# Kernel optimization log

Hardware: AMD Instinct MI355X
Metric: run time of the kernel (lower is better)

## Reference

```python
import jax, jax.numpy as jnp
import numpy as np

N_NODES = 50000
N_EDGES = 1200000
N_REL = 40
N_BASES = 30
EMB = 64
HID = 128
N_GRAPHS = 64


def rgcn_layer(h, src, dst, edge_type, comp, basis, root, bias):
    # W_r = sum_b comp[r,b] * basis[b]  -> [R, in, out]
    W = jnp.einsum('rb,bio->rio', comp, basis)
    n = h.shape[0]
    # aggregate source features per (target node, relation): mean aggregation (PyG RGCNConv default)
    seg = dst * N_REL + edge_type                      # [E]
    msgs = h[src]                                      # [E, in]  (gather)
    agg = jax.ops.segment_sum(msgs, seg, num_segments=n * N_REL)
    agg = agg.reshape(n, N_REL, -1)                    # [N, R, in]
    cnt = jax.ops.segment_sum(jnp.ones((src.shape[0],), h.dtype), seg,
                              num_segments=n * N_REL).reshape(n, N_REL, 1)
    agg = agg / jnp.maximum(cnt, 1.0)
    out = jnp.einsum('nri,rio->no', agg, W) + h @ root + bias
    return out


def setup_inputs() -> dict:
    key = jax.random.key(0)
    ks = jax.random.split(key, 12)
    x = jnp.arange(N_NODES, dtype=jnp.int64) if jax.config.jax_enable_x64 else jnp.arange(N_NODES, dtype=jnp.int32)
    edge_index = jax.random.randint(ks[0], (2, N_EDGES), 0, N_NODES)
    edge_type = jax.random.randint(ks[1], (N_EDGES,), 0, N_REL)
    batch = jnp.sort(jax.random.randint(ks[2], (N_NODES,), 0, N_GRAPHS))
    s = 0.05
    node_emb = jax.random.normal(ks[3], (N_NODES, EMB), jnp.float32)
    comp1 = jax.random.normal(ks[4], (N_REL, N_BASES), jnp.float32) * s
    basis1 = jax.random.normal(ks[5], (N_BASES, EMB, HID), jnp.float32) * s
    root1 = jax.random.normal(ks[6], (EMB, HID), jnp.float32) * s
    bias1 = jnp.zeros((HID,), jnp.float32)
    comp2 = jax.random.normal(ks[7], (N_REL, N_BASES), jnp.float32) * s
    basis2 = jax.random.normal(ks[8], (N_BASES, HID, HID), jnp.float32) * s
    root2 = jax.random.normal(ks[9], (HID, HID), jnp.float32) * s
    bias2 = jnp.zeros((HID,), jnp.float32)
    return {"x": x, "edge_index": edge_index, "edge_type": edge_type, "batch": batch,
            "node_emb": node_emb,
            "comp1": comp1, "basis1": basis1, "root1": root1, "bias1": bias1,
            "comp2": comp2, "basis2": basis2, "root2": root2, "bias2": bias2}


def reference(x, edge_index, edge_type, batch, node_emb,
              comp1, basis1, root1, bias1, comp2, basis2, root2, bias2):
    src, dst = edge_index[0], edge_index[1]
    h = node_emb[x]                                              # embedding lookup
    h = jax.nn.relu(rgcn_layer(h, src, dst, edge_type, comp1, basis1, root1, bias1))
    h = jax.nn.relu(rgcn_layer(h, src, dst, edge_type, comp2, basis2, root2, bias2))
    # global mean pool over graphs in batch
    sums = jax.ops.segment_sum(h, batch, num_segments=N_GRAPHS)  # [G, HID]
    cnts = jax.ops.segment_sum(jnp.ones((h.shape[0],), h.dtype), batch,
                               num_segments=N_GRAPHS)[:, None]
    return sums / jnp.maximum(cnts, 1.0)
```

## Files before the change

### kernel.cpp

```cpp
#include <hip/hip_runtime.h>


#define N_NODES 50000
#define N_EDGES 1200000
#define N_REL   40
#define N_BASES 30
#define EMB     64
#define HID     128
#define N_GRAPHS 64

#define NKEY      320
#define PERM_CAP  ((size_t)N_EDGES + (size_t)NKEY * 256)
#define SP_EPB    1024

typedef float f32x4  __attribute__((ext_vector_type(4)));
typedef short bf16x8 __attribute__((ext_vector_type(8)));

__device__ __forceinline__ unsigned short f2bf(float x) {
    unsigned int u = __float_as_uint(x);
    u = (u + 0x7FFFu + ((u >> 16) & 1u)) >> 16;
    return (unsigned short)u;
}
__device__ __forceinline__ float bflo(unsigned int u) { return __uint_as_float(u << 16); }
__device__ __forceinline__ float bfhi(unsigned int u) { return __uint_as_float(u & 0xffff0000u); }

#define OFF_WF1   ((size_t)0)
#define OFF_WF2   ((size_t)163840)
#define OFF_CNT   ((size_t)491520)
#define OFF_H1    ((size_t)2491520)
#define OFF_H2    ((size_t)8891520)
#define OFF_HB1   ((size_t)15291520)
#define OFF_HB2   ((size_t)16891520)
#define OFF_CNTG  ((size_t)20091520)
#define OFF_POOL  ((size_t)20091584)
#define OFF_PSRC  ((size_t)20099776)
#define OFF_POS   ((size_t)21381696)
#define OFF_PDST  ((size_t)22663616)
#define OFF_HCR   ((size_t)23945536)
#define OFF_CCR   ((size_t)23945856)
#define OFF_POCR  ((size_t)23946176)
#define OFF_HD    ((size_t)23946560)
#define OFF_CD    ((size_t)23996560)
#define OFF_POD   ((size_t)24046560)
#define OFF_RF1   ((size_t)24096576)
#define OFF_RF2   ((size_t)24100672)
#define OFF_BREL  ((size_t)24108864)
#define OFF_PM    ((size_t)24110912)

template <int IN, int KT>
__global__ void k_Wfrag(const float* __restrict__ comp, const float* __restrict__ basis,
                        unsigned short* __restrict__ Wf) {
    const int FR = IN * HID;
    int idx = blockIdx.x * blockDim.x + threadIdx.x;
    if (idx >= N_REL * FR) return;
    int r = idx / FR, F = idx - r * FR;
    int j = F & 7, lane = (F >> 3) & 63, tt = F >> 9;
    int kt = tt % KT, ct = tt / KT;
    int k = kt * 32 + (lane >> 4) * 8 + j;
    int c = ct * 16 + (lane & 15);
    float s = 0.f;
#pragma unroll
    for (int b = 0; b < N_BASES; ++b)
        s += comp[r * N_BASES + b] * basis[((size_t)b * IN + k) * HID + c];
    Wf[idx] = f2bf(s);
}

template <int IN, int KT>
__global__ void k_rootfrag(const float* __restrict__ root, unsigned short* __restrict__ rf) {
    int idx = blockIdx.x * blockDim.x + threadIdx.x;
    if (idx >= IN * HID) return;
    int j = idx & 7, lane = (idx >> 3) & 63, tt = idx >> 9;
    int kt = tt % KT, ct = tt / KT;
    int k = kt * 32 + (lane >> 4) * 8 + j;
    int c = ct * 16 + (lane & 15);
    rf[idx] = f2bf(root[k * HID + c]);
}

__global__ void k_count(const int* __restrict__ dst, const int* __restrict__ etype,
                        float* __restrict__ cnt_t) {
    int e = blockIdx.x * blockDim.x + threadIdx.x;
    if (e >= N_EDGES) return;
    atomicAdd(&cnt_t[(size_t)etype[e] * N_NODES + dst[e]], 1.0f);
}

__global__ void k_deg_inv(float* __restrict__ cnt_t, int* __restrict__ hist) {
    int n = blockIdx.x * blockDim.x + threadIdx.x;
    if (n >= N_NODES) return;
    float s = 0.f;
#pragma unroll 8
    for (int r = 0; r < N_REL; ++r) {
        float c = cnt_t[(size_t)r * N_NODES + n];
        s += c;
        cnt_t[(size_t)r * N_NODES + n] = 1.0f / fmaxf(c, 1.0f);
    }
    hist[n] = (int)(s + 0.5f);
}

__global__ void k_scan_d(const int* __restrict__ hist, int* __restrict__ po) {
    __shared__ int csum[256];
    int t = threadIdx.x;
    const int CH = (N_NODES + 255) / 256;
    int k0 = t * CH, k1 = min(k0 + CH, N_NODES);
    int s = 0;
    for (int k = k0; k < k1; ++k) s += hist[k];
    csum[t] = s;
    __syncthreads();
    if (t == 0) {
        int acc = 0;
        for (int i = 0; i < 256; ++i) { int v = csum[i]; csum[i] = acc; acc += v; }
        po[N_NODES] = acc;
    }
    __syncthreads();
    int base = csum[t];
    for (int k = k0; k < k1; ++k) { po[k] = base; base += hist[k]; }
}

__global__ void k_hist_cr(const int* __restrict__ src, const int* __restrict__ dst,
                          const int* __restrict__ etype, int* __restrict__ hist,
                          int chn, int slc, int sdiv) {
    __shared__ int lh[NKEY];
    for (int t = threadIdx.x; t < NKEY; t += 256) lh[t] = 0;
    __syncthreads();
    int e = blockIdx.x * blockDim.x + threadIdx.x;
    if (e < N_EDGES) {
        int key = (dst[e] / chn) * (N_REL * slc) + etype[e] * slc + src[e] / sdiv;
        atomicAdd(&lh[key], 1);
    }
    __syncthreads();
    for (int t = threadIdx.x; t < NKEY; t += 256)
        if (lh[t]) atomicAdd(&hist[t], lh[t]);
}

__global__ void k_scan_cr(const int* __restrict__ hist, int* __restrict__ po) {
    if (threadIdx.x == 0) {
        int acc = 0;
        for (int k = 0; k < NKEY; ++k) {
            po[k] = acc;
            acc += ((hist[k] + 255) >> 8) << 8;
        }
        po[NKEY] = acc;
    }
}

__global__ void k_brel(const int* __restrict__ po, unsigned char* __restrict__ brel,
                       int slc) {
    int k = blockIdx.x * blockDim.x + threadIdx.x;
    if (k >= NKEY) return;
    unsigned char r = (unsigned char)((k % (N_REL * slc)) / slc);
    for (int b = po[k] >> 8; b < (po[k + 1] >> 8); ++b) brel[b] = r;
}

__global__ void k_fillpads(const int* __restrict__ hist, const int* __restrict__ po,
                           int* __restrict__ ps_src, int* __restrict__ ps_os,
                           int* __restrict__ ps_dst, int dumprow) {
    int k = blockIdx.x;
    int start = po[k] + hist[k], end = po[k + 1];
    for (int s = start + threadIdx.x; s < end; s += blockDim.x) {
        ps_src[s] = 0;
        ps_os[s] = dumprow;
        ps_dst[s] = 0;
    }
}

__global__ void k_scatter_s(const int* __restrict__ src, const int* __restrict__ dst,
                            const int* __restrict__ etype,
                            const int* __restrict__ po_cr, int* __restrict__ cur_cr,
                            const int* __restrict__ po_d, int* __restrict__ cur_d,
                            int* __restrict__ ps_src, int* __restrict__ ps_os,
                            int* __restrict__ ps_dst, int chn, int slc, int sdiv) {
    __shared__ int lh[NKEY], sbase[NKEY];
    int t = threadIdx.x;
    for (int k = t; k < NKEY; k += 256) lh[k] = 0;
    __syncthreads();
    int e0 = blockIdx.x * SP_EPB;
    int e_[4], key_[4];
#pragma unroll
    for (int i = 0; i < 4; ++i) {
        int e = e0 + t + i * 256;
        e_[i] = e;
        if (e < N_EDGES) {
            key_[i] = (dst[e] / chn) * (N_REL * slc) + etype[e] * slc + src[e] / sdiv;
            atomicAdd(&lh[key_[i]], 1);
        }
    }
    __syncthreads();
    for (int k = t; k < NKEY; k += 256) {
        if (lh[k]) sbase[k] = atomicAdd(&cur_cr[k], lh[k]);
        lh[k] = 0;
    }
    __syncthreads();
#pragma unroll
    for (int i = 0; i < 4; ++i) {
        if (e_[i] < N_EDGES) {
            int e = e_[i], key = key_[i];
            int d = dst[e];
            int p = atomicAdd(&lh[key], 1);
            int slot = po_cr[key] + sbase[key] + p;
            int os_g = po_d[d] + atomicAdd(&cur_d[d], 1);
            int os_l = os_g - po_d[(d / chn) * chn];
            ps_src[slot] = src[e];
            ps_os[slot] = os_l;
            ps_dst[slot] = d;
        }
    }
}

template <int IN, int KT>
__global__ __launch_bounds__(256, 4)
void k_rootgemm(const unsigned short* __restrict__ hb_in,
                const unsigned short* __restrict__ rf,
                const float* __restrict__ bias, float* __restrict__ h) {
    __shared__ unsigned short Wl[8 * KT * 64 * 8];
    {
        const f32x4* Wg = (const f32x4*)rf;
        f32x4* Wd = (f32x4*)Wl;
        for (int kk = threadIdx.x; kk < 8 * KT * 64; kk += 256) Wd[kk] = Wg[kk];
    }
    __syncthreads();

    int l = threadIdx.x & 63, wv = threadIdx.x >> 6;
    int lrow = l & 15, lk = l >> 4;
    int nbase = blockIdx.x * 64 + wv * 16;

    int nrow = min(nbase + lrow, N_NODES - 1);
    bf16x8 a[KT];
    const unsigned short* hrow = hb_in + (size_t)nrow * IN + lk * 8;
#pragma unroll
    for (int kt = 0; kt < KT; ++kt)
        a[kt] = *(const bf16x8*)(hrow + kt * 32);

    f32x4 acc[8];
#pragma unroll
    for (int ct = 0; ct < 8; ++ct) acc[ct] = (f32x4){0.f, 0.f, 0.f, 0.f};
#pragma unroll
    for (int ct = 0; ct < 8; ++ct) {
#pragma unroll
        for (int kt = 0; kt < KT; ++kt) {
            bf16x8 bb = *(const bf16x8*)(Wl + ((ct * KT + kt) * 64 + l) * 8);
            acc[ct] = __builtin_amdgcn_mfma_f32_16x16x32_bf16(a[kt], bb, acc[ct], 0, 0, 0);
        }
    }
#pragma unroll
    for (int q = 0; q < 4; ++q) {
        int n = nbase + lk * 4 + q;
        if (n < N_NODES) {
#pragma unroll
            for (int ct = 0; ct < 8; ++ct)
                h[(size_t)n * HID + ct * 16 + lrow] = acc[ct][q] + bias[ct * 16 + lrow];
        }
    }
}

template <int IN, int KT>
__global__ __launch_bounds__(256, 4)
void k_msg(const unsigned short* __restrict__ hb_in, const int* __restrict__ ps_src,
           const int* __restrict__ ps_os, const int* __restrict__ ps_dst,
           const float* __restrict__ invc_t, const int* __restrict__ pob, int nbk,
           const unsigned char* __restrict__ brel,
           const unsigned short* __restrict__ Wf, unsigned int* __restrict__ pm) {
    __shared__ unsigned short Wl[8 * KT * 64 * 8];
    int slot0 = pob[0] + blockIdx.x * 256;
    if (slot0 >= pob[nbk]) return;
    int r = brel[slot0 >> 8];

    {
        const f32x4* Wg = (const f32x4*)(Wf + (size_t)r * (8 * KT * 64 * 8));
        f32x4* Wd = (f32x4*)Wl;
        for (int kk = threadIdx.x; kk < 8 * KT * 64; kk += 256) Wd[kk] = Wg[kk];
    }
    __syncthreads();

    int l = threadIdx.x & 63, wv = threadIdx.x >> 6;
    int lrow = l & 15, lk = l >> 4;
    const float* invr = invc_t + (size_t)r * N_NODES;

    for (int t = wv; t < 16; t += 4) {
        int slot = slot0 + t * 16 + lrow;
        int sv = ps_src[slot];
        int os = ps_os[slot];
        int d  = ps_dst[slot];
        float inv = invr[d];

        bf16x8 a[KT];
        const unsigned short* hrow = hb_in + (size_t)sv * IN + lk * 8;
#pragma unroll
        for (int kt = 0; kt < KT; ++kt)
            a[kt] = *(const bf16x8*)(hrow + kt * 32);

        f32x4 acc[8];
#pragma unroll
        for (int ct = 0; ct < 8; ++ct) acc[ct] = (f32x4){0.f, 0.f, 0.f, 0.f};
#pragma unroll
        for (int ct = 0; ct < 8; ++ct) {
#pragma unroll
            for (int kt = 0; kt < KT; ++kt) {
                bf16x8 bb = *(const bf16x8*)(Wl + ((ct * KT + kt) * 64 + l) * 8);
                acc[ct] = __builtin_amdgcn_mfma_f32_16x16x32_bf16(a[kt], bb, acc[ct], 0, 0, 0);
            }
        }
#pragma unroll
        for (int q = 0; q < 4; ++q) {
            int row = lk * 4 + q;
            int osq   = __shfl(os, row);
            float ivq = __shfl(inv, row);
            unsigned int* dp = pm + (size_t)osq * 64 + lrow;
#pragma unroll
            for (int cp = 0; cp < 4; ++cp) {
                unsigned int u = (unsigned int)f2bf(acc[2 * cp][q] * ivq)
                               | ((unsigned int)f2bf(acc[2 * cp + 1][q] * ivq) << 16);
                dp[cp * 16] = u;
            }
        }
    }
}

template <bool WRITE_HB>
__global__ __launch_bounds__(256, 8)
void k_reduce(const unsigned int* __restrict__ pm, const int* __restrict__ po_d,
              int n0chunk, int chn, float* __restrict__ h,
              unsigned short* __restrict__ hb_out) {
    int wv = threadIdx.x >> 6, p = threadIdx.x & 63;
    int n = n0chunk + blockIdx.x * 4 + wv;
    if (n >= n0chunk + chn) return;
    int pmbase = po_d[n0chunk];
    int b0 = po_d[n] - pmbase;
    int cn = po_d[n + 1] - pmbase - b0;
    float lo = 0.f, hi = 0.f;
    const unsigned int* rp = pm + (size_t)b0 * 64 + p;
    int k = 0;
    for (; k + 4 <= cn; k += 4) {
        unsigned int u0 = rp[0], u1 = rp[64], u2 = rp[128], u3 = rp[192];
        rp += 256;
        lo += bflo(u0) + bflo(u1) + bflo(u2) + bflo(u3);
        hi += bfhi(u0) + bfhi(u1) + bfhi(u2) + bfhi(u3);
    }
    for (; k < cn; ++k) {
        unsigned int u = rp[0];
        rp += 64;
        lo += bflo(u); hi += bfhi(u);
    }
    int cA = (p & 15) + 32 * (p >> 4);
    float* hp = h + (size_t)n * HID;
    float vA = fmaxf(hp[cA] + lo, 0.f);
    float vB = fmaxf(hp[cA + 16] + hi, 0.f);
    hp[cA] = vA;
    hp[cA + 16] = vB;
    if (WRITE_HB) {
        hb_out[(size_t)n * HID + cA] = f2bf(vA);
        hb_out[(size_t)n * HID + cA + 16] = f2bf(vB);
    }
}

__global__ void k_cvt_emb(const float* __restrict__ emb, const int* __restrict__ x,
                          unsigned short* __restrict__ hb) {
    int idx = blockIdx.x * blockDim.x + threadIdx.x;
    if (idx >= N_NODES * (EMB / 4)) return;
    int n = idx / (EMB / 4), c4 = idx % (EMB / 4);
    int row = x[n];
    float4 v = *(const float4*)(emb + (size_t)row * EMB + c4 * 4);
    ushort4 o = {f2bf(v.x), f2bf(v.y), f2bf(v.z), f2bf(v.w)};
    *(ushort4*)(hb + (size_t)n * EMB + c4 * 4) = o;
}

__global__ void k_gcount2(const int* __restrict__ batch, float* __restrict__ cntG) {
    int g = threadIdx.x;
    if (g >= N_GRAPHS) return;
    int lo = 0, hi = N_NODES;
    while (lo < hi) { int m = (lo + hi) >> 1; if (batch[m] < g) lo = m + 1; else hi = m; }
    int lb0 = lo;
    lo = 0; hi = N_NODES;
    while (lo < hi) { int m = (lo + hi) >> 1; if (batch[m] < g + 1) lo = m + 1; else hi = m; }
    cntG[g] = (float)(lo - lb0);
}

__global__ void k_pool(const float* __restrict__ h, const int* __restrict__ batch,
                       float* __restrict__ acc) {
    const int CH = 64;
    int n0 = blockIdx.x * CH;
    int o = threadIdx.x;
    int nend = min(n0 + CH, N_NODES);
    if (n0 >= N_NODES) return;
    int curg = batch[n0];
    float run = 0.f;
    for (int n = n0; n < nend; ++n) {
        int g = batch[n];
        if (g != curg) {
            atomicAdd(&acc[(size_t)curg * HID + o], run);
            run = 0.f;
            curg = g;
        }
        run += h[(size_t)n * HID + o];
    }
    atomicAdd(&acc[(size_t)curg * HID + o], run);
}

__global__ void k_final(const float* __restrict__ acc, const float* __restrict__ cntG,
                        float* __restrict__ out) {
    int idx = blockIdx.x * blockDim.x + threadIdx.x;
    if (idx >= N_GRAPHS * HID) return;
    int g = idx >> 7;
    out[idx] = acc[idx] / fmaxf(cntG[g], 1.0f);
}

extern "C" void kernel_launch(void* const* d_in, const int* in_sizes, int n_in,
                              void* d_out, int out_size, void* d_ws, size_t ws_size,
                              hipStream_t stream) {
    const int*   x         = (const int*)d_in[0];
    const int*   edge_index= (const int*)d_in[1];
    const int*   etype     = (const int*)d_in[2];
    const int*   batch     = (const int*)d_in[3];
    const float* node_emb  = (const float*)d_in[4];
    const float* comp1     = (const float*)d_in[5];
    const float* basis1    = (const float*)d_in[6];
    const float* root1     = (const float*)d_in[7];
    const float* bias1     = (const float*)d_in[8];
    const float* comp2     = (const float*)d_in[9];
    const float* basis2    = (const float*)d_in[10];
    const float* root2     = (const float*)d_in[11];
    const float* bias2     = (const float*)d_in[12];
    float* out = (float*)d_out;

    const int* src = edge_index;
    const int* dst = edge_index + N_EDGES;

    float* ws = (float*)d_ws;
    unsigned short* Wf1 = (unsigned short*)(ws + OFF_WF1);
    unsigned short* Wf2 = (unsigned short*)(ws + OFF_WF2);
    float* cnt_t = ws + OFF_CNT;
    float* h1   = ws + OFF_H1;
    float* h2   = ws + OFF_H2;
    unsigned short* hb1 = (unsigned short*)(ws + OFF_HB1);
    unsigned short* hb2 = (unsigned short*)(ws + OFF_HB2);
    float* cntG = ws + OFF_CNTG;
    float* pool = ws + OFF_POOL;
    int*   ps_src = (int*)(ws + OFF_PSRC);
    int*   ps_os  = (int*)(ws + OFF_POS);
    int*   ps_dst = (int*)(ws + OFF_PDST);
    int*   hist_cr = (int*)(ws + OFF_HCR);
    int*   cur_cr  = (int*)(ws + OFF_CCR);
    int*   po_cr   = (int*)(ws + OFF_POCR);
    int*   hist_d  = (int*)(ws + OFF_HD);
    int*   cur_d   = (int*)(ws + OFF_CD);
    int*   po_d    = (int*)(ws + OFF_POD);
    unsigned short* rf1 = (unsigned short*)(ws + OFF_RF1);
    unsigned short* rf2 = (unsigned short*)(ws + OFF_RF2);
    unsigned char* brel = (unsigned char*)(ws + OFF_BREL);
    unsigned int* pm = (unsigned int*)(ws + OFF_PM);

    size_t ws_floats = ws_size / sizeof(float);
    int nch = 4;
    if (ws_floats >= OFF_PM + ((size_t)N_EDGES / 1 + 12504) * 64) nch = 1;
    else if (ws_floats >= OFF_PM + ((size_t)N_EDGES / 2 + 12504) * 64) nch = 2;
    int chn = N_NODES / nch;
    int slc = 8 / nch;
    int sdiv = 6250 * nch;
    int nbk = NKEY / nch;
    int capr = N_EDGES / nch + 12504;
    int gridm = (capr + NKEY * 256 / nch) / 256 + 2;

    hipMemsetAsync(cnt_t, 0, (size_t)N_NODES * N_REL * sizeof(float), stream);
    hipMemsetAsync(cntG, 0, (size_t)(N_GRAPHS + N_GRAPHS * HID) * sizeof(float), stream);
    hipMemsetAsync(hist_cr, 0, 2 * NKEY * sizeof(int), stream);
    hipMemsetAsync(cur_d, 0, N_NODES * sizeof(int), stream);

    k_count<<<(N_EDGES + 255) / 256, 256, 0, stream>>>(dst, etype, cnt_t);
    k_deg_inv<<<(N_NODES + 255) / 256, 256, 0, stream>>>(cnt_t, hist_d);
    k_scan_d<<<1, 256, 0, stream>>>(hist_d, po_d);
    k_hist_cr<<<(N_EDGES + 255) / 256, 256, 0, stream>>>(src, dst, etype, hist_cr,
                                                         chn, slc, sdiv);
    k_scan_cr<<<1, 64, 0, stream>>>(hist_cr, po_cr);
    k_brel<<<2, 256, 0, stream>>>(po_cr, brel, slc);
    k_fillpads<<<NKEY, 256, 0, stream>>>(hist_cr, po_cr, ps_src, ps_os, ps_dst, capr - 1);
    k_scatter_s<<<(N_EDGES + SP_EPB - 1) / SP_EPB, 256, 0, stream>>>(
        src, dst, etype, po_cr, cur_cr, po_d, cur_d, ps_src, ps_os, ps_dst,
        chn, slc, sdiv);

    k_Wfrag<EMB, 2><<<(N_REL * EMB * HID + 255) / 256, 256, 0, stream>>>(comp1, basis1, Wf1);
    k_Wfrag<HID, 4><<<(N_REL * HID * HID + 255) / 256, 256, 0, stream>>>(comp2, basis2, Wf2);
    k_rootfrag<EMB, 2><<<(EMB * HID + 255) / 256, 256, 0, stream>>>(root1, rf1);
    k_rootfrag<HID, 4><<<(HID * HID + 255) / 256, 256, 0, stream>>>(root2, rf2);

    k_cvt_emb<<<(N_NODES * (EMB / 4) + 255) / 256, 256, 0, stream>>>(node_emb, x, hb1);
    k_rootgemm<EMB, 2><<<(N_NODES + 63) / 64, 256, 0, stream>>>(hb1, rf1, bias1, h1);
    for (int c = 0; c < nch; ++c) {
        k_msg<EMB, 2><<<gridm, 256, 0, stream>>>(hb1, ps_src, ps_os, ps_dst, cnt_t,
                                                 po_cr + c * nbk, nbk, brel, Wf1, pm);
        k_reduce<true><<<chn / 4, 256, 0, stream>>>(pm, po_d, c * chn, chn, h1, hb2);
    }

    k_rootgemm<HID, 4><<<(N_NODES + 63) / 64, 256, 0, stream>>>(hb2, rf2, bias2, h2);
    for (int c = 0; c < nch; ++c) {
        k_msg<HID, 4><<<gridm, 256, 0, stream>>>(hb2, ps_src, ps_os, ps_dst, cnt_t,
                                                 po_cr + c * nbk, nbk, brel, Wf2, pm);
        k_reduce<false><<<chn / 4, 256, 0, stream>>>(pm, po_d, c * chn, chn, h2, nullptr);
    }

    k_gcount2<<<1, 64, 0, stream>>>(batch, cntG);
    k_pool<<<(N_NODES + 63) / 64, HID, 0, stream>>>(h2, batch, pool);
    k_final<<<(N_GRAPHS * HID + 255) / 256, 256, 0, stream>>>(pool, cntG, out);
}
```

Before: 1.068 ms.

## Reorder message-block schedule by source slice via block map, add nontemporal pm traffic

Bucket keys are reorganized so the source-slice index is the outer dimension when a single chunk is used, and a new block map permutes the message blocks. Consecutive blocks then walk relations within the same source slice, which aims to keep the gathered source rows resident in cache. Pad filling becomes one grid-stride fill of the whole permutation buffer. The partial-message stores and the reduce loads now use nontemporal hints to keep streaming data out of the cache. The trade is an extra mapping kernel, a larger fill pass, and an indirect lookup per block.

```diff
diff --git a/kernel.cpp b/kernel.cpp
--- a/kernel.cpp
+++ b/kernel.cpp
@@ -9,9 +9,10 @@
 #define HID     128
 #define N_GRAPHS 64
 
-#define NKEY      320
-#define PERM_CAP  ((size_t)N_EDGES + (size_t)NKEY * 256)
+#define NKEY_MAX  320
+#define PERM_CAP  ((size_t)N_EDGES + (size_t)NKEY_MAX * 256)
 #define SP_EPB    1024
+#define SLW       6250
 
 typedef float f32x4  __attribute__((ext_vector_type(4)));
 typedef short bf16x8 __attribute__((ext_vector_type(8)));
@@ -45,7 +46,8 @@
 #define OFF_RF1   ((size_t)24096576)
 #define OFF_RF2   ((size_t)24100672)
 #define OFF_BREL  ((size_t)24108864)
-#define OFF_PM    ((size_t)24110912)
+#define OFF_BMAP  ((size_t)24110912)
+#define OFF_PM    ((size_t)24119104)
 
 template <int IN, int KT>
 __global__ void k_Wfrag(const float* __restrict__ comp, const float* __restrict__ basis,
@@ -115,47 +117,75 @@
     for (int k = k0; k < k1; ++k) { po[k] = base; base += hist[k]; }
 }
 
+__device__ __forceinline__ int bucket_key(int d, int s, int r, int chn, int nbk, int slc) {
+    int key = (d / chn) * nbk + r;
+    if (slc == 8) key += (s / SLW) * N_REL;
+    return key;
+}
+
 __global__ void k_hist_cr(const int* __restrict__ src, const int* __restrict__ dst,
                           const int* __restrict__ etype, int* __restrict__ hist,
-                          int chn, int slc, int sdiv) {
-    __shared__ int lh[NKEY];
-    for (int t = threadIdx.x; t < NKEY; t += 256) lh[t] = 0;
+                          int chn, int nbk, int slc) {
+    __shared__ int lh[NKEY_MAX];
+    for (int t = threadIdx.x; t < NKEY_MAX; t += 256) lh[t] = 0;
     __syncthreads();
     int e = blockIdx.x * blockDim.x + threadIdx.x;
-    if (e < N_EDGES) {
-        int key = (dst[e] / chn) * (N_REL * slc) + etype[e] * slc + src[e] / sdiv;
-        atomicAdd(&lh[key], 1);
-    }
-    __syncthreads();
-    for (int t = threadIdx.x; t < NKEY; t += 256)
+    if (e < N_EDGES)
+        atomicAdd(&lh[bucket_key(dst[e], src[e], etype[e], chn, nbk, slc)], 1);
+    __syncthreads();
+    for (int t = threadIdx.x; t < NKEY_MAX; t += 256)
         if (lh[t]) atomicAdd(&hist[t], lh[t]);
 }
 
-__global__ void k_scan_cr(const int* __restrict__ hist, int* __restrict__ po) {
+__global__ void k_scan_cr(const int* __restrict__ hist, int* __restrict__ po, int nkeyc) {
     if (threadIdx.x == 0) {
         int acc = 0;
-        for (int k = 0; k < NKEY; ++k) {
+        for (int k = 0; k < nkeyc; ++k) {
             po[k] = acc;
             acc += ((hist[k] + 255) >> 8) << 8;
         }
-        po[NKEY] = acc;
+        po[nkeyc] = acc;
     }
 }
 
 __global__ void k_brel(const int* __restrict__ po, unsigned char* __restrict__ brel,
-                       int slc) {
+                       int nkeyc) {
     int k = blockIdx.x * blockDim.x + threadIdx.x;
-    if (k >= NKEY) return;
-    unsigned char r = (unsigned char)((k % (N_REL * slc)) / slc);
+    if (k >= nkeyc) return;
+    unsigned char r = (unsigned char)(k % N_REL);
     for (int b = po[k] >> 8; b < (po[k + 1] >> 8); ++b) brel[b] = r;
 }
 
-__global__ void k_fillpads(const int* __restrict__ hist, const int* __restrict__ po,
-                           int* __restrict__ ps_src, int* __restrict__ ps_os,
-                           int* __restrict__ ps_dst, int dumprow) {
-    int k = blockIdx.x;
-    int start = po[k] + hist[k], end = po[k + 1];
-    for (int s = start + threadIdx.x; s < end; s += blockDim.x) {
+__global__ void k_bmap(const int* __restrict__ po, int nch, int nbk, int slc,
+                       int* __restrict__ bmap) {
+    int g = blockIdx.x * blockDim.x + threadIdx.x;
+    int total = po[nch * nbk] >> 8;
+    if (g >= total) return;
+    int c = 0;
+    while ((po[(c + 1) * nbk] >> 8) <= g) ++c;
+    int cb0 = po[c * nbk] >> 8;
+    int j = g - cb0;
+    if (slc != 8) { bmap[g] = j; return; }
+    int B[9];
+#pragma unroll
+    for (int s = 0; s <= 8; ++s) B[s] = (po[c * nbk + s * N_REL] >> 8) - cb0;
+    int s = 0;
+    while (B[s + 1] <= j) ++s;
+    int jj = j - B[s];
+    int p = 0;
+#pragma unroll
+    for (int t = 0; t < 8; ++t) {
+        int sz = B[t + 1] - B[t];
+        p += min(jj, sz);
+        if (t < s && sz > jj) ++p;
+    }
+    bmap[cb0 + p] = j;
+}
+
+__global__ void k_fill(int* __restrict__ ps_src, int* __restrict__ ps_os,
+                       int* __restrict__ ps_dst, int dumprow) {
+    for (size_t s = (size_t)blockIdx.x * blockDim.x + threadIdx.x; s < PERM_CAP;
+         s += (size_t)gridDim.x * blockDim.x) {
         ps_src[s] = 0;
         ps_os[s] = dumprow;
         ps_dst[s] = 0;
@@ -167,10 +197,10 @@
                             const int* __restrict__ po_cr, int* __restrict__ cur_cr,
                             const int* __restrict__ po_d, int* __restrict__ cur_d,
                             int* __restrict__ ps_src, int* __restrict__ ps_os,
-                            int* __restrict__ ps_dst, int chn, int slc, int sdiv) {
-    __shared__ int lh[NKEY], sbase[NKEY];
+                            int* __restrict__ ps_dst, int chn, int nbk, int slc) {
+    __shared__ int lh[NKEY_MAX], sbase[NKEY_MAX];
     int t = threadIdx.x;
-    for (int k = t; k < NKEY; k += 256) lh[k] = 0;
+    for (int k = t; k < NKEY_MAX; k += 256) lh[k] = 0;
     __syncthreads();
     int e0 = blockIdx.x * SP_EPB;
     int e_[4], key_[4];
@@ -179,12 +209,12 @@
         int e = e0 + t + i * 256;
         e_[i] = e;
         if (e < N_EDGES) {
-            key_[i] = (dst[e] / chn) * (N_REL * slc) + etype[e] * slc + src[e] / sdiv;
+            key_[i] = bucket_key(dst[e], src[e], etype[e], chn, nbk, slc);
             atomicAdd(&lh[key_[i]], 1);
         }
     }
     __syncthreads();
-    for (int k = t; k < NKEY; k += 256) {
+    for (int k = t; k < NKEY_MAX; k += 256) {
         if (lh[k]) sbase[k] = atomicAdd(&cur_cr[k], lh[k]);
         lh[k] = 0;
     }
@@ -255,12 +285,16 @@
 __global__ __launch_bounds__(256, 4)
 void k_msg(const unsigned short* __restrict__ hb_in, const int* __restrict__ ps_src,
            const int* __restrict__ ps_os, const int* __restrict__ ps_dst,
-           const float* __restrict__ invc_t, const int* __restrict__ pob, int nbk,
-           const unsigned char* __restrict__ brel,
+           const float* __restrict__ invc_t,
+           const int* __restrict__ po_c, int nbk,
+           const unsigned char* __restrict__ brel, const int* __restrict__ bmap,
            const unsigned short* __restrict__ Wf, unsigned int* __restrict__ pm) {
     __shared__ unsigned short Wl[8 * KT * 64 * 8];
-    int slot0 = pob[0] + blockIdx.x * 256;
-    if (slot0 >= pob[nbk]) return;
+    int base = po_c[0];
+    int total = (po_c[nbk] - base) >> 8;
+    if (blockIdx.x >= total) return;
+    int myblk = bmap[(base >> 8) + blockIdx.x];
+    int slot0 = base + myblk * 256;
     int r = brel[slot0 >> 8];
 
     {
@@ -308,7 +342,7 @@
             for (int cp = 0; cp < 4; ++cp) {
                 unsigned int u = (unsigned int)f2bf(acc[2 * cp][q] * ivq)
                                | ((unsigned int)f2bf(acc[2 * cp + 1][q] * ivq) << 16);
-                dp[cp * 16] = u;
+                __builtin_nontemporal_store(u, dp + cp * 16);
             }
         }
     }
@@ -329,13 +363,16 @@
     const unsigned int* rp = pm + (size_t)b0 * 64 + p;
     int k = 0;
     for (; k + 4 <= cn; k += 4) {
-        unsigned int u0 = rp[0], u1 = rp[64], u2 = rp[128], u3 = rp[192];
+        unsigned int u0 = __builtin_nontemporal_load(rp);
+        unsigned int u1 = __builtin_nontemporal_load(rp + 64);
+        unsigned int u2 = __builtin_nontemporal_load(rp + 128);
+        unsigned int u3 = __builtin_nontemporal_load(rp + 192);
         rp += 256;
         lo += bflo(u0) + bflo(u1) + bflo(u2) + bflo(u3);
         hi += bfhi(u0) + bfhi(u1) + bfhi(u2) + bfhi(u3);
     }
     for (; k < cn; ++k) {
-        unsigned int u = rp[0];
+        unsigned int u = __builtin_nontemporal_load(rp);
         rp += 64;
         lo += bflo(u); hi += bfhi(u);
     }
@@ -445,6 +482,7 @@
     unsigned short* rf1 = (unsigned short*)(ws + OFF_RF1);
     unsigned short* rf2 = (unsigned short*)(ws + OFF_RF2);
     unsigned char* brel = (unsigned char*)(ws + OFF_BREL);
+    int*   bmap = (int*)(ws + OFF_BMAP);
     unsigned int* pm = (unsigned int*)(ws + OFF_PM);
 
     size_t ws_floats = ws_size / sizeof(float);
@@ -452,28 +490,30 @@
     if (ws_floats >= OFF_PM + ((size_t)N_EDGES / 1 + 12504) * 64) nch = 1;
     else if (ws_floats >= OFF_PM + ((size_t)N_EDGES / 2 + 12504) * 64) nch = 2;
     int chn = N_NODES / nch;
-    int slc = 8 / nch;
-    int sdiv = 6250 * nch;
-    int nbk = NKEY / nch;
+    int slc = (nch == 1) ? 8 : 1;
+    int nbk = slc * N_REL;
+    int nkeyc = nch * nbk;
     int capr = N_EDGES / nch + 12504;
-    int gridm = (capr + NKEY * 256 / nch) / 256 + 2;
+    int gridm = (capr + 255) / 256 + nbk + 2;
+    int totblk_max = (int)(PERM_CAP >> 8) + 1;
 
     hipMemsetAsync(cnt_t, 0, (size_t)N_NODES * N_REL * sizeof(float), stream);
     hipMemsetAsync(cntG, 0, (size_t)(N_GRAPHS + N_GRAPHS * HID) * sizeof(float), stream);
-    hipMemsetAsync(hist_cr, 0, 2 * NKEY * sizeof(int), stream);
+    hipMemsetAsync(hist_cr, 0, 2 * NKEY_MAX * sizeof(int), stream);
     hipMemsetAsync(cur_d, 0, N_NODES * sizeof(int), stream);
 
     k_count<<<(N_EDGES + 255) / 256, 256, 0, stream>>>(dst, etype, cnt_t);
     k_deg_inv<<<(N_NODES + 255) / 256, 256, 0, stream>>>(cnt_t, hist_d);
     k_scan_d<<<1, 256, 0, stream>>>(hist_d, po_d);
     k_hist_cr<<<(N_EDGES + 255) / 256, 256, 0, stream>>>(src, dst, etype, hist_cr,
-                                                         chn, slc, sdiv);
-    k_scan_cr<<<1, 64, 0, stream>>>(hist_cr, po_cr);
-    k_brel<<<2, 256, 0, stream>>>(po_cr, brel, slc);
-    k_fillpads<<<NKEY, 256, 0, stream>>>(hist_cr, po_cr, ps_src, ps_os, ps_dst, capr - 1);
+                                                         chn, nbk, slc);
+    k_scan_cr<<<1, 64, 0, stream>>>(hist_cr, po_cr, nkeyc);
+    k_brel<<<2, 256, 0, stream>>>(po_cr, brel, nkeyc);
+    k_bmap<<<(totblk_max + 255) / 256, 256, 0, stream>>>(po_cr, nch, nbk, slc, bmap);
+    k_fill<<<2048, 256, 0, stream>>>(ps_src, ps_os, ps_dst, capr - 1);
     k_scatter_s<<<(N_EDGES + SP_EPB - 1) / SP_EPB, 256, 0, stream>>>(
         src, dst, etype, po_cr, cur_cr, po_d, cur_d, ps_src, ps_os, ps_dst,
-        chn, slc, sdiv);
+        chn, nbk, slc);
 
     k_Wfrag<EMB, 2><<<(N_REL * EMB * HID + 255) / 256, 256, 0, stream>>>(comp1, basis1, Wf1);
     k_Wfrag<HID, 4><<<(N_REL * HID * HID + 255) / 256, 256, 0, stream>>>(comp2, basis2, Wf2);
@@ -484,14 +524,16 @@
     k_rootgemm<EMB, 2><<<(N_NODES + 63) / 64, 256, 0, stream>>>(hb1, rf1, bias1, h1);
     for (int c = 0; c < nch; ++c) {
         k_msg<EMB, 2><<<gridm, 256, 0, stream>>>(hb1, ps_src, ps_os, ps_dst, cnt_t,
-                                                 po_cr + c * nbk, nbk, brel, Wf1, pm);
+                                                 po_cr + c * nbk, nbk, brel, bmap,
+                                                 Wf1, pm);
         k_reduce<true><<<chn / 4, 256, 0, stream>>>(pm, po_d, c * chn, chn, h1, hb2);
     }
 
     k_rootgemm<HID, 4><<<(N_NODES + 63) / 64, 256, 0, stream>>>(hb2, rf2, bias2, h2);
     for (int c = 0; c < nch; ++c) {
         k_msg<HID, 4><<<gridm, 256, 0, stream>>>(hb2, ps_src, ps_os, ps_dst, cnt_t,
-                                                 po_cr + c * nbk, nbk, brel, Wf2, pm);
+                                                 po_cr + c * nbk, nbk, brel, bmap,
+                                                 Wf2, pm);
         k_reduce<false><<<chn / 4, 256, 0, stream>>>(pm, po_d, c * chn, chn, h2, nullptr);
     }
 
```

Measured after the change: 1.033 ms. 1.03x faster.
